# Kernel tuning notes

Hardware: AMD Instinct MI355X
Metric: run time of the kernel (lower is better)

## Reference

```python
import jax, jax.numpy as jnp
import numpy as np

N_NODES = 87381  # complete 4-ary tree of depth 9: (4**9 - 1) / 3
VOCAB = 32000
D_IN = 256
M_DIM = 256


def setup_inputs() -> dict:
    key = jax.random.key(0)
    ks = jax.random.split(key, 10)
    w = lambda k, s: jax.random.normal(k, s, dtype=jnp.float32) * 0.05
    return {
        "tokens": jax.random.randint(ks[0], (N_NODES,), 0, VOCAB),
        "branching": 4,
        "emb": w(ks[1], (VOCAB, D_IN)),
        "Wioux": w(ks[2], (D_IN, 3 * M_DIM)),
        "bioux": w(ks[3], (3 * M_DIM,)),
        "Wiouh": w(ks[4], (M_DIM, 3 * M_DIM)),
        "biouh": w(ks[5], (3 * M_DIM,)),
        "Wfx": w(ks[6], (D_IN, M_DIM)),
        "bfx": w(ks[7], (M_DIM,)),
        "Wfh": w(ks[8], (M_DIM, M_DIM)),
        "bfh": w(ks[9], (M_DIM,)),
    }


def _levels(n, b):
    # BFS level boundaries (start, size) for a complete b-ary tree with n nodes
    out, start, size = [], 0, 1
    while start < n:
        out.append((start, min(size, n - start)))
        start += size
        size *= b
    return out


def reference(tokens, branching, emb, Wioux, bioux, Wiouh, biouh, Wfx, bfx, Wfh, bfh):
    N = tokens.shape[0]
    b = int(branching)
    M = Wfh.shape[0]
    x = emb[tokens]                       # [N, D_IN] per-node inputs
    xiou = x @ Wioux + bioux              # [N, 3M] precomputed input gate terms
    xf = x @ Wfx + bfx                    # [N, M]
    h = jnp.zeros((N, M), x.dtype)
    c = jnp.zeros((N, M), x.dtype)
    for (s, sz) in reversed(_levels(N, b)):  # leaves -> root
        idx = jnp.arange(s, s + sz)
        child = idx[:, None] * b + 1 + jnp.arange(b)[None, :]   # [sz, b]
        valid = (child < N)[..., None].astype(x.dtype)          # [sz, b, 1]
        ci = jnp.where(child < N, child, 0)
        ch = h[ci] * valid                                      # [sz, b, M]
        cc = c[ci] * valid
        iou = xiou[idx] + ch.sum(axis=1) @ Wiouh + biouh        # [sz, 3M]
        i, o, u = jnp.split(iou, 3, axis=1)
        i, o, u = jax.nn.sigmoid(i), jax.nn.sigmoid(o), jnp.tanh(u)
        f = jax.nn.sigmoid(ch @ Wfh + bfh + xf[idx][:, None, :])  # [sz, b, M]
        c_new = i * u + jnp.sum(f * cc * valid, axis=1)
        h_new = o * jnp.tanh(c_new)
        c = c.at[idx].set(c_new)
        h = h.at[idx].set(h_new)
    return h  # hidden state of every node; root state is h[0]
```

## Files before the change

### kernel.cpp

```cpp
#include <hip/hip_runtime.h>
#include <cstdint>
#include <cstddef>

typedef _Float16 f16;
typedef __attribute__((ext_vector_type(8))) _Float16 half8;
typedef __attribute__((ext_vector_type(4))) _Float16 half4;
typedef __attribute__((ext_vector_type(8))) short short8;
typedef __attribute__((ext_vector_type(4))) float floatx4;
typedef __attribute__((ext_vector_type(8))) float floatx8;

__device__ __forceinline__ float rcp_(float x) { return __builtin_amdgcn_rcpf(x); }
__device__ __forceinline__ float sigm(float x) { return rcp_(1.f + __expf(-x)); }
__device__ __forceinline__ float tanh_(float x) { return 1.f - 2.f * rcp_(1.f + __expf(2.f * x)); }

__global__ __launch_bounds__(256) void gemm128d(
    const f16* __restrict__ A0, const f16* __restrict__ B0, f16* __restrict__ C0,
    int ldc0, int nt0, int tiles0,
    const f16* __restrict__ A1, const f16* __restrict__ B1, f16* __restrict__ C1,
    int ldc1, int nt1)
{
  const f16* A; const f16* BT; f16* C; int ldc_, mi, ni;
  int bid = blockIdx.x;
  if (bid < tiles0) { A = A0; BT = B0; C = C0; ldc_ = ldc0; mi = bid / nt0; ni = bid % nt0; }
  else { int r = bid - tiles0; A = A1; BT = B1; C = C1; ldc_ = ldc1; mi = r / nt1; ni = r % nt1; }
  const int m0 = mi * 128;
  const int n0 = ni * 128;

  __shared__ short lA[128 * 72];
  __shared__ short lB[128 * 72];
  const int t = threadIdx.x;
  const int wave = t >> 6;
  const int lane = t & 63;
  const int ln = lane & 15;
  const int quad = lane >> 4;
  const int wr = wave >> 1;
  const int wc = wave & 1;

  floatx4 acc[4][4];
#pragma unroll
  for (int i = 0; i < 4; ++i)
#pragma unroll
    for (int j = 0; j < 4; ++j) acc[i][j] = (floatx4){0.f, 0.f, 0.f, 0.f};

#pragma unroll
  for (int st = 0; st < 4; ++st) {
    const int k0 = st * 64;
#pragma unroll
    for (int i = 0; i < 4; ++i) {
      int chunk = t + 256 * i;
      int row = chunk >> 3;
      int cc = chunk & 7;
      *(short8*)&lA[row * 72 + cc * 8] =
          *(const short8*)(A + (size_t)(m0 + row) * 256 + k0 + cc * 8);
      *(short8*)&lB[row * 72 + cc * 8] =
          *(const short8*)(BT + (size_t)(n0 + row) * 256 + k0 + cc * 8);
    }
    __syncthreads();
#pragma unroll
    for (int ks = 0; ks < 2; ++ks) {
      const int kk = ks * 32 + quad * 8;
      half8 a[4], b[4];
#pragma unroll
      for (int rf = 0; rf < 4; ++rf)
        a[rf] = __builtin_bit_cast(half8,
            *(const short8*)&lA[(wr * 64 + rf * 16 + ln) * 72 + kk]);
#pragma unroll
      for (int cf = 0; cf < 4; ++cf)
        b[cf] = __builtin_bit_cast(half8,
            *(const short8*)&lB[(wc * 64 + cf * 16 + ln) * 72 + kk]);
#pragma unroll
      for (int rf = 0; rf < 4; ++rf)
#pragma unroll
        for (int cf = 0; cf < 4; ++cf)
          acc[rf][cf] = __builtin_amdgcn_mfma_f32_16x16x32_f16(
              a[rf], b[cf], acc[rf][cf], 0, 0, 0);
    }
    __syncthreads();
  }
#pragma unroll
  for (int rf = 0; rf < 4; ++rf)
#pragma unroll
    for (int cf = 0; cf < 4; ++cf)
#pragma unroll
      for (int r = 0; r < 4; ++r) {
        int row = m0 + wr * 64 + rf * 16 + quad * 4 + r;
        int col = n0 + wc * 64 + cf * 16 + ln;
        C[(size_t)row * ldc_ + col] = (f16)acc[rf][cf][r];
      }
}

__global__ __launch_bounds__(256) void prep(
    const float* __restrict__ emb, const float* __restrict__ Wioux,
    const float* __restrict__ Wfx, const float* __restrict__ Wiouh,
    const float* __restrict__ Wfh,
    f16* __restrict__ emb_h, f16* __restrict__ BTX,
    f16* __restrict__ WiouhT, f16* __restrict__ WfhT)
{
  int idx = blockIdx.x * 256 + threadIdx.x;
  if (idx < 2048000) {
    floatx4 v = *(const floatx4*)(emb + 4 * (size_t)idx);
    half4 o;
#pragma unroll
    for (int j = 0; j < 4; ++j) o[j] = (f16)v[j];
    *(half4*)(emb_h + 4 * (size_t)idx) = o;
  } else if (idx < 2310144) {
    int r = idx - 2048000;
    int j = r >> 8, k = r & 255;
    BTX[r] = (f16)((j < 768) ? Wioux[(size_t)k * 768 + j]
                             : Wfx[(size_t)k * 256 + (j - 768)]);
  } else if (idx < 2506752) {
    int r = idx - 2310144;
    int j = r >> 8, k = r & 255;
    WiouhT[r] = (f16)Wiouh[(size_t)k * 768 + j];
  } else {
    int r = idx - 2506752;
    int j = r >> 8, k = r & 255;
    WfhT[r] = (f16)Wfh[(size_t)k * 256 + j];
  }
}

__global__ __launch_bounds__(256) void elem8(
    const int* __restrict__ tokens, const f16* __restrict__ TIOUF,
    const f16* __restrict__ IOUH, const f16* __restrict__ FH,
    const float* __restrict__ bioux, const float* __restrict__ biouh,
    const float* __restrict__ bfx, const float* __restrict__ bfh,
    f16* __restrict__ c16, float* __restrict__ h, f16* __restrict__ h16,
    f16* __restrict__ hsum16, int s, int sz, int s_up, int sz_up, int leaf)
{
  __shared__ float hsh[8 * 260];
  const int t = threadIdx.x;
  const int nloc = t >> 5;
  const int d0 = (t & 31) * 8;
  const int base = s + 8 * blockIdx.x;
  const int node = base + nloc;
  const int lim = s + sz;

  if (node < lim) {
    const f16* ti = TIOUF + (size_t)tokens[node] * 1024;
    half8 t0 = *(const half8*)(ti + d0);
    half8 t1 = *(const half8*)(ti + 256 + d0);
    half8 t2 = *(const half8*)(ti + 512 + d0);
    floatx8 bi0 = *(const floatx8*)(bioux + d0) + *(const floatx8*)(biouh + d0);
    floatx8 bi1 = *(const floatx8*)(bioux + 256 + d0) + *(const floatx8*)(biouh + 256 + d0);
    floatx8 bi2 = *(const floatx8*)(bioux + 512 + d0) + *(const floatx8*)(biouh + 512 + d0);

    float cv[8];
    if (leaf) {
#pragma unroll
      for (int j = 0; j < 8; ++j)
        cv[j] = sigm((float)t0[j] + bi0[j]) * tanh_((float)t2[j] + bi2[j]);
    } else {
      const f16* io = IOUH + (size_t)(node - s) * 768;
      half8 io0 = *(const half8*)(io + d0);
      half8 io1 = *(const half8*)(io + 256 + d0);
      half8 io2 = *(const half8*)(io + 512 + d0);
      half8 t3 = *(const half8*)(ti + 768 + d0);
      floatx8 bff = *(const floatx8*)(bfx + d0) + *(const floatx8*)(bfh + d0);
      size_t ch = 4 * (size_t)node + 1;
      half8 fh0 = *(const half8*)(FH + (ch + 0) * 256 + d0);
      half8 fh1 = *(const half8*)(FH + (ch + 1) * 256 + d0);
      half8 fh2 = *(const half8*)(FH + (ch + 2) * 256 + d0);
      half8 fh3 = *(const half8*)(FH + (ch + 3) * 256 + d0);
      half8 cc0 = *(const half8*)(c16 + (ch + 0) * 256 + d0);
      half8 cc1 = *(const half8*)(c16 + (ch + 1) * 256 + d0);
      half8 cc2 = *(const half8*)(c16 + (ch + 2) * 256 + d0);
      half8 cc3 = *(const half8*)(c16 + (ch + 3) * 256 + d0);
#pragma unroll
      for (int j = 0; j < 8; ++j) {
        float xff = (float)t3[j] + bff[j];
        float v = sigm((float)t0[j] + (float)io0[j] + bi0[j]) *
                  tanh_((float)t2[j] + (float)io2[j] + bi2[j]);
        v += sigm((float)fh0[j] + xff) * (float)cc0[j];
        v += sigm((float)fh1[j] + xff) * (float)cc1[j];
        v += sigm((float)fh2[j] + xff) * (float)cc2[j];
        v += sigm((float)fh3[j] + xff) * (float)cc3[j];
        cv[j] = v;
      }
      t1 = __builtin_bit_cast(half8,
           __builtin_bit_cast(short8, t1));
#pragma unroll
      for (int j = 0; j < 8; ++j) bi1[j] += (float)io1[j];
    }

    half8 c8, h8;
    floatx8 hf;
#pragma unroll
    for (int j = 0; j < 8; ++j) {
      float hv = sigm((float)t1[j] + bi1[j]) * tanh_(cv[j]);
      c8[j] = (f16)cv[j];
      h8[j] = (f16)hv;
      hf[j] = hv;
    }
    *(half8*)(c16 + (size_t)node * 256 + d0) = c8;
    *(floatx8*)(h + (size_t)node * 256 + d0) = hf;
    *(half8*)(h16 + (size_t)node * 256 + d0) = h8;
    *(floatx8*)&hsh[nloc * 260 + d0] = hf;
  }
  __syncthreads();

  if (s_up >= 0 && t < 64) {
    int p = t >> 5;
    int dd = (t & 31) * 8;
    int parent = ((base - 1) >> 2) + p;
    if (parent < s_up + sz_up) {
      floatx8 v = *(const floatx8*)&hsh[(4 * p + 0) * 260 + dd] +
                  *(const floatx8*)&hsh[(4 * p + 1) * 260 + dd] +
                  *(const floatx8*)&hsh[(4 * p + 2) * 260 + dd] +
                  *(const floatx8*)&hsh[(4 * p + 3) * 260 + dd];
      half8 o;
#pragma unroll
      for (int j = 0; j < 8; ++j) o[j] = (f16)v[j];
      *(half8*)(hsum16 + (size_t)(parent - s_up) * 256 + dd) = o;
    }
  }
}

__global__ __launch_bounds__(512) void fused_level(
    const int* __restrict__ tokens, const f16* __restrict__ TIOUF,
    const f16* __restrict__ WiouhT, const f16* __restrict__ WfhT,
    const float* __restrict__ bioux, const float* __restrict__ biouh,
    const float* __restrict__ bfx, const float* __restrict__ bfh,
    f16* __restrict__ c16, float* __restrict__ h, f16* __restrict__ h16,
    const f16* __restrict__ hsum_in, f16* __restrict__ hsum_out,
    int s, int sz, int sz_up)
{
  __shared__ short lA[80 * 264];
  __shared__ float lFS[8][16][17];
  __shared__ int ltok[16];

  const int t = threadIdx.x;
  const int pt = blockIdx.x >> 1;
  const int pg = blockIdx.x & 1;
  const int p0 = s + pt * 16;
  const int c0 = 4 * p0 + 1;

  if (t < 16) ltok[t] = tokens[p0 + t];
#pragma unroll
  for (int i = 0; i < 5; ++i) {
    int chunk = t + 512 * i;
    int row = chunk >> 5;
    int cc = chunk & 31;
    const f16* src = (row < 16)
        ? hsum_in + (size_t)(pt * 16 + row) * 256 + cc * 8
        : h16 + (size_t)(c0 + row - 16) * 256 + cc * 8;
    *(short8*)&lA[row * 264 + cc * 8] = *(const short8*)src;
  }
  __syncthreads();

  const int wave = t >> 6;
  const int lane = t & 63;
  const int ln = lane & 15;
  const int q = lane >> 4;
  const int dim = (pg * 8 + wave) * 16 + ln;

  floatx4 accI[3], accF[4];
#pragma unroll
  for (int i = 0; i < 3; ++i) accI[i] = (floatx4){0.f, 0.f, 0.f, 0.f};
#pragma unroll
  for (int i = 0; i < 4; ++i) accF[i] = (floatx4){0.f, 0.f, 0.f, 0.f};

  const short* aH = &lA[ln * 264 + 8 * q];
  const short* aC = &lA[(16 + ln) * 264 + 8 * q];
  const f16* b0p = WiouhT + (size_t)dim * 256 + 8 * q;
  const f16* b1p = WiouhT + (size_t)(256 + dim) * 256 + 8 * q;
  const f16* b2p = WiouhT + (size_t)(512 + dim) * 256 + 8 * q;
  const f16* bfp = WfhT + (size_t)dim * 256 + 8 * q;

#pragma unroll
  for (int ks = 0; ks < 8; ++ks) {
    const int ko = 32 * ks;
    half8 ah = __builtin_bit_cast(half8, *(const short8*)(aH + ko));
    half8 b0 = *(const half8*)(b0p + ko);
    half8 b1 = *(const half8*)(b1p + ko);
    half8 b2 = *(const half8*)(b2p + ko);
    half8 bf = *(const half8*)(bfp + ko);
    accI[0] = __builtin_amdgcn_mfma_f32_16x16x32_f16(ah, b0, accI[0], 0, 0, 0);
    accI[1] = __builtin_amdgcn_mfma_f32_16x16x32_f16(ah, b1, accI[1], 0, 0, 0);
    accI[2] = __builtin_amdgcn_mfma_f32_16x16x32_f16(ah, b2, accI[2], 0, 0, 0);
#pragma unroll
    for (int rt = 0; rt < 4; ++rt) {
      half8 ac = __builtin_bit_cast(half8,
          *(const short8*)(aC + rt * (16 * 264) + ko));
      accF[rt] = __builtin_amdgcn_mfma_f32_16x16x32_f16(ac, bf, accF[rt], 0, 0, 0);
    }
  }

  const float bi0 = bioux[dim] + biouh[dim];
  const float bi1 = bioux[256 + dim] + biouh[256 + dim];
  const float bi2 = bioux[512 + dim] + biouh[512 + dim];
  const float bff = bfx[dim] + bfh[dim];

#pragma unroll
  for (int rt = 0; rt < 4; ++rt) {
    int po = 4 * rt + q;
    float xff = (float)TIOUF[(size_t)ltok[po] * 1024 + 768 + dim] + bff;
    float fs = 0.f;
#pragma unroll
    for (int r = 0; r < 4; ++r) {
      size_t child = (size_t)(c0 + 16 * rt + 4 * q + r);
      fs += sigm(accF[rt][r] + xff) * (float)c16[child * 256 + dim];
    }
    lFS[wave][po][ln] = fs;
  }
  __syncthreads();

  const int szrem = sz - pt * 16;
  float hsum = 0.f;
#pragma unroll
  for (int r = 0; r < 4; ++r) {
    int po = 4 * q + r;
    const f16* tp = TIOUF + (size_t)ltok[po] * 1024;
    float iv = sigm(accI[0][r] + (float)tp[dim] + bi0);
    float ov = sigm(accI[1][r] + (float)tp[256 + dim] + bi1);
    float uv = tanh_(accI[2][r] + (float)tp[512 + dim] + bi2);
    float cn = iv * uv + lFS[wave][po][ln];
    float hn = ov * tanh_(cn);
    hsum += hn;
    if (po < szrem) {
      size_t pi = (size_t)(p0 + po);
      c16[pi * 256 + dim] = (f16)cn;
      h16[pi * 256 + dim] = (f16)hn;
      h[pi * 256 + dim] = hn;
    }
  }
  if (hsum_out) {
    int g_row = 4 * pt + q;
    if (g_row < sz_up)
      hsum_out[(size_t)g_row * 256 + dim] = (f16)hsum;
  }
}

extern "C" void kernel_launch(void* const* d_in, const int* in_sizes, int n_in,
                              void* d_out, int out_size, void* d_ws, size_t ws_size,
                              hipStream_t stream) {
  const int*   tokens = (const int*)d_in[0];
  const float* emb    = (const float*)d_in[2];
  const float* Wioux  = (const float*)d_in[3];
  const float* bioux  = (const float*)d_in[4];
  const float* Wiouh  = (const float*)d_in[5];
  const float* biouh  = (const float*)d_in[6];
  const float* Wfx    = (const float*)d_in[7];
  const float* bfx    = (const float*)d_in[8];
  const float* Wfh    = (const float*)d_in[9];
  const float* bfh    = (const float*)d_in[10];
  float* h = (float*)d_out;
  (void)in_sizes; (void)n_in; (void)out_size; (void)ws_size;

  f16* emb_h   = (f16*)d_ws;
  f16* BTX     = emb_h   + 8192000;
  f16* WiouhT  = BTX     + 262144;
  f16* WfhT    = WiouhT  + 196608;
  f16* TIOUF   = WfhT    + 65536;
  f16* hsumB   = TIOUF   + (size_t)32768000;
  f16* FH_dead = hsumB   + (size_t)12582912;
  f16* h16     = FH_dead + (size_t)22396928;
  f16* hsumA   = h16     + (size_t)22396928;
  f16* c16     = hsumA   + (size_t)4194304;

  prep<<<10049, 256, 0, stream>>>(emb, Wioux, Wfx, Wiouh, Wfh,
                                  emb_h, BTX, WiouhT, WfhT);

  gemm128d<<<2000, 256, 0, stream>>>(emb_h, BTX, TIOUF, 1024, 8, 2000,
                                     emb_h, BTX, TIOUF, 1024, 8);

  const int LV[9][2] = {{21845, 65536}, {5461, 16384}, {1365, 4096},
                        {341, 1024},    {85, 256},     {21, 64},
                        {5, 16},        {1, 4},        {0, 1}};

  elem8<<<8192, 256, 0, stream>>>(tokens, TIOUF, nullptr, nullptr,
                                  bioux, biouh, bfx, bfh,
                                  c16, h, h16, hsumA, 21845, 65536, 5461, 16384, 1);

  for (int i = 1; i < 9; ++i) {
    int s = LV[i][0], sz = LV[i][1];
    int sz_up = (i < 8) ? LV[i + 1][1] : 0;
    const f16* hin = (i & 1) ? hsumA : hsumB;
    f16* hout = (i < 8) ? ((i & 1) ? hsumB : hsumA) : nullptr;
    int blocks = 2 * ((sz + 15) / 16);
    fused_level<<<blocks, 512, 0, stream>>>(
        tokens, TIOUF, WiouhT, WfhT, bioux, biouh, bfx, bfh,
        c16, h, h16, hin, hout, s, sz, sz_up);
  }
}
```

Measured before the change: 387.5 us.

## Prefetch child cell states and token gate terms into LDS, double-buffer weight loads

Before the MFMA loop, fused_level now issues coalesced loads of the children's c16 values and the parents' TIOUF gate rows, then stages them in LDS after the GEMM. This replaces the scattered per-element global reads in the epilogue. Weight fragments are software-pipelined one k-step ahead, and the launch bounds request two blocks per CU. The unused non-leaf path in elem8 is also removed. The cost is more live registers and extra barriers.

```diff
diff --git a/kernel.cpp b/kernel.cpp
--- a/kernel.cpp
+++ b/kernel.cpp
@@ -121,11 +121,9 @@
 
 __global__ __launch_bounds__(256) void elem8(
     const int* __restrict__ tokens, const f16* __restrict__ TIOUF,
-    const f16* __restrict__ IOUH, const f16* __restrict__ FH,
     const float* __restrict__ bioux, const float* __restrict__ biouh,
-    const float* __restrict__ bfx, const float* __restrict__ bfh,
     f16* __restrict__ c16, float* __restrict__ h, f16* __restrict__ h16,
-    f16* __restrict__ hsum16, int s, int sz, int s_up, int sz_up, int leaf)
+    f16* __restrict__ hsum16, int s, int sz, int s_up, int sz_up)
 {
   __shared__ float hsh[8 * 260];
   const int t = threadIdx.x;
@@ -145,42 +143,9 @@
     floatx8 bi2 = *(const floatx8*)(bioux + 512 + d0) + *(const floatx8*)(biouh + 512 + d0);
 
     float cv[8];
-    if (leaf) {
-#pragma unroll
-      for (int j = 0; j < 8; ++j)
-        cv[j] = sigm((float)t0[j] + bi0[j]) * tanh_((float)t2[j] + bi2[j]);
-    } else {
-      const f16* io = IOUH + (size_t)(node - s) * 768;
-      half8 io0 = *(const half8*)(io + d0);
-      half8 io1 = *(const half8*)(io + 256 + d0);
-      half8 io2 = *(const half8*)(io + 512 + d0);
-      half8 t3 = *(const half8*)(ti + 768 + d0);
-      floatx8 bff = *(const floatx8*)(bfx + d0) + *(const floatx8*)(bfh + d0);
-      size_t ch = 4 * (size_t)node + 1;
-      half8 fh0 = *(const half8*)(FH + (ch + 0) * 256 + d0);
-      half8 fh1 = *(const half8*)(FH + (ch + 1) * 256 + d0);
-      half8 fh2 = *(const half8*)(FH + (ch + 2) * 256 + d0);
-      half8 fh3 = *(const half8*)(FH + (ch + 3) * 256 + d0);
-      half8 cc0 = *(const half8*)(c16 + (ch + 0) * 256 + d0);
-      half8 cc1 = *(const half8*)(c16 + (ch + 1) * 256 + d0);
-      half8 cc2 = *(const half8*)(c16 + (ch + 2) * 256 + d0);
-      half8 cc3 = *(const half8*)(c16 + (ch + 3) * 256 + d0);
-#pragma unroll
-      for (int j = 0; j < 8; ++j) {
-        float xff = (float)t3[j] + bff[j];
-        float v = sigm((float)t0[j] + (float)io0[j] + bi0[j]) *
-                  tanh_((float)t2[j] + (float)io2[j] + bi2[j]);
-        v += sigm((float)fh0[j] + xff) * (float)cc0[j];
-        v += sigm((float)fh1[j] + xff) * (float)cc1[j];
-        v += sigm((float)fh2[j] + xff) * (float)cc2[j];
-        v += sigm((float)fh3[j] + xff) * (float)cc3[j];
-        cv[j] = v;
-      }
-      t1 = __builtin_bit_cast(half8,
-           __builtin_bit_cast(short8, t1));
-#pragma unroll
-      for (int j = 0; j < 8; ++j) bi1[j] += (float)io1[j];
-    }
+#pragma unroll
+    for (int j = 0; j < 8; ++j)
+      cv[j] = sigm((float)t0[j] + bi0[j]) * tanh_((float)t2[j] + bi2[j]);
 
     half8 c8, h8;
     floatx8 hf;
@@ -198,7 +163,7 @@
   }
   __syncthreads();
 
-  if (s_up >= 0 && t < 64) {
+  if (t < 64) {
     int p = t >> 5;
     int dd = (t & 31) * 8;
     int parent = ((base - 1) >> 2) + p;
@@ -215,7 +180,7 @@
   }
 }
 
-__global__ __launch_bounds__(512) void fused_level(
+__global__ __launch_bounds__(512, 2) void fused_level(
     const int* __restrict__ tokens, const f16* __restrict__ TIOUF,
     const f16* __restrict__ WiouhT, const f16* __restrict__ WfhT,
     const float* __restrict__ bioux, const float* __restrict__ biouh,
@@ -226,7 +191,6 @@
 {
   __shared__ short lA[80 * 264];
   __shared__ float lFS[8][16][17];
-  __shared__ int ltok[16];
 
   const int t = threadIdx.x;
   const int pt = blockIdx.x >> 1;
@@ -234,7 +198,7 @@
   const int p0 = s + pt * 16;
   const int c0 = 4 * p0 + 1;
 
-  if (t < 16) ltok[t] = tokens[p0 + t];
+  short8 sA[5];
 #pragma unroll
   for (int i = 0; i < 5; ++i) {
     int chunk = t + 512 * i;
@@ -243,7 +207,22 @@
     const f16* src = (row < 16)
         ? hsum_in + (size_t)(pt * 16 + row) * 256 + cc * 8
         : h16 + (size_t)(c0 + row - 16) * 256 + cc * 8;
-    *(short8*)&lA[row * 264 + cc * 8] = *(const short8*)src;
+    sA[i] = *(const short8*)src;
+  }
+  const int tok0 = tokens[p0 + (t >> 6)];
+  const int tok1 = tokens[p0 + (t >> 6) + 8];
+  short8 pre[4];
+  pre[0] = *(const short8*)(c16 + (size_t)(c0 + (t >> 4)) * 256 + pg * 128 + (t & 15) * 8);
+  pre[1] = *(const short8*)(c16 + (size_t)(c0 + 32 + (t >> 4)) * 256 + pg * 128 + (t & 15) * 8);
+  pre[2] = *(const short8*)(TIOUF + (size_t)tok0 * 1024 + ((t >> 4) & 3) * 256 + pg * 128 + (t & 15) * 8);
+  pre[3] = *(const short8*)(TIOUF + (size_t)tok1 * 1024 + ((t >> 4) & 3) * 256 + pg * 128 + (t & 15) * 8);
+
+#pragma unroll
+  for (int i = 0; i < 5; ++i) {
+    int chunk = t + 512 * i;
+    int row = chunk >> 5;
+    int cc = chunk & 31;
+    *(short8*)&lA[row * 264 + cc * 8] = sA[i];
   }
   __syncthreads();
 
@@ -266,14 +245,21 @@
   const f16* b2p = WiouhT + (size_t)(512 + dim) * 256 + 8 * q;
   const f16* bfp = WfhT + (size_t)dim * 256 + 8 * q;
 
+  half8 b0 = *(const half8*)(b0p);
+  half8 b1 = *(const half8*)(b1p);
+  half8 b2 = *(const half8*)(b2p);
+  half8 bf = *(const half8*)(bfp);
 #pragma unroll
   for (int ks = 0; ks < 8; ++ks) {
     const int ko = 32 * ks;
+    half8 n0, n1, n2, nf;
+    if (ks < 7) {
+      n0 = *(const half8*)(b0p + ko + 32);
+      n1 = *(const half8*)(b1p + ko + 32);
+      n2 = *(const half8*)(b2p + ko + 32);
+      nf = *(const half8*)(bfp + ko + 32);
+    }
     half8 ah = __builtin_bit_cast(half8, *(const short8*)(aH + ko));
-    half8 b0 = *(const half8*)(b0p + ko);
-    half8 b1 = *(const half8*)(b1p + ko);
-    half8 b2 = *(const half8*)(b2p + ko);
-    half8 bf = *(const half8*)(bfp + ko);
     accI[0] = __builtin_amdgcn_mfma_f32_16x16x32_f16(ah, b0, accI[0], 0, 0, 0);
     accI[1] = __builtin_amdgcn_mfma_f32_16x16x32_f16(ah, b1, accI[1], 0, 0, 0);
     accI[2] = __builtin_amdgcn_mfma_f32_16x16x32_f16(ah, b2, accI[2], 0, 0, 0);
@@ -283,8 +269,19 @@
           *(const short8*)(aC + rt * (16 * 264) + ko));
       accF[rt] = __builtin_amdgcn_mfma_f32_16x16x32_f16(ac, bf, accF[rt], 0, 0, 0);
     }
-  }
-
+    b0 = n0; b1 = n1; b2 = n2; bf = nf;
+  }
+
+  __syncthreads();
+  short* lR = lA;
+  short* lTb = lA + 64 * 134;
+  *(short8*)&lR[(t >> 4) * 134 + (t & 15) * 8] = pre[0];
+  *(short8*)&lR[(32 + (t >> 4)) * 134 + (t & 15) * 8] = pre[1];
+  *(short8*)&lTb[(t >> 4) * 134 + (t & 15) * 8] = pre[2];
+  *(short8*)&lTb[(32 + (t >> 4)) * 134 + (t & 15) * 8] = pre[3];
+  __syncthreads();
+
+  const int dl = wave * 16 + ln;
   const float bi0 = bioux[dim] + biouh[dim];
   const float bi1 = bioux[256 + dim] + biouh[256 + dim];
   const float bi2 = bioux[512 + dim] + biouh[512 + dim];
@@ -293,12 +290,12 @@
 #pragma unroll
   for (int rt = 0; rt < 4; ++rt) {
     int po = 4 * rt + q;
-    float xff = (float)TIOUF[(size_t)ltok[po] * 1024 + 768 + dim] + bff;
+    float xff = (float)__builtin_bit_cast(f16, lTb[(po * 4 + 3) * 134 + dl]) + bff;
     float fs = 0.f;
 #pragma unroll
     for (int r = 0; r < 4; ++r) {
-      size_t child = (size_t)(c0 + 16 * rt + 4 * q + r);
-      fs += sigm(accF[rt][r] + xff) * (float)c16[child * 256 + dim];
+      float ccv = (float)__builtin_bit_cast(f16, lR[(16 * rt + 4 * q + r) * 134 + dl]);
+      fs += sigm(accF[rt][r] + xff) * ccv;
     }
     lFS[wave][po][ln] = fs;
   }
@@ -309,10 +306,12 @@
 #pragma unroll
   for (int r = 0; r < 4; ++r) {
     int po = 4 * q + r;
-    const f16* tp = TIOUF + (size_t)ltok[po] * 1024;
-    float iv = sigm(accI[0][r] + (float)tp[dim] + bi0);
-    float ov = sigm(accI[1][r] + (float)tp[256 + dim] + bi1);
-    float uv = tanh_(accI[2][r] + (float)tp[512 + dim] + bi2);
+    float t0v = (float)__builtin_bit_cast(f16, lTb[(po * 4 + 0) * 134 + dl]);
+    float t1v = (float)__builtin_bit_cast(f16, lTb[(po * 4 + 1) * 134 + dl]);
+    float t2v = (float)__builtin_bit_cast(f16, lTb[(po * 4 + 2) * 134 + dl]);
+    float iv = sigm(accI[0][r] + t0v + bi0);
+    float ov = sigm(accI[1][r] + t1v + bi1);
+    float uv = tanh_(accI[2][r] + t2v + bi2);
     float cn = iv * uv + lFS[wave][po][ln];
     float hn = ov * tanh_(cn);
     hsum += hn;
@@ -367,9 +366,8 @@
                         {341, 1024},    {85, 256},     {21, 64},
                         {5, 16},        {1, 4},        {0, 1}};
 
-  elem8<<<8192, 256, 0, stream>>>(tokens, TIOUF, nullptr, nullptr,
-                                  bioux, biouh, bfx, bfh,
-                                  c16, h, h16, hsumA, 21845, 65536, 5461, 16384, 1);
+  elem8<<<8192, 256, 0, stream>>>(tokens, TIOUF, bioux, biouh,
+                                  c16, h, h16, hsumA, 21845, 65536, 5461, 16384);
 
   for (int i = 1; i < 9; ++i) {
     int s = LV[i][0], sz = LV[i][1];
```

Result: no change. 388.1 us (+0.2%).
